# Optimization experiments

Measured on AMD Instinct MI355X. Metric: run time of the kernel, lower is better.

The kernel has to match this reference:

```python
import jax, jax.numpy as jnp
import numpy as np

NUM_HEADS = 16
HEAD_SIZE = 64
D_MODEL = NUM_HEADS * HEAD_SIZE  # 1024


def setup_inputs() -> dict:
    key = jax.random.key(0)
    ks = jax.random.split(key, 12)
    B, S = 4, 2048
    q = jax.random.normal(ks[0], (B, S, D_MODEL), dtype=jnp.float32)
    k = jax.random.normal(ks[1], (B, S, D_MODEL), dtype=jnp.float32)
    v = jax.random.normal(ks[2], (B, S, D_MODEL), dtype=jnp.float32)
    w = jax.random.uniform(ks[3], (B, S), dtype=jnp.float32)
    scale = 1.0 / np.sqrt(D_MODEL)
    Wq = jax.random.normal(ks[4], (D_MODEL, D_MODEL), dtype=jnp.float32) * scale
    Wk = jax.random.normal(ks[5], (D_MODEL, D_MODEL), dtype=jnp.float32) * scale
    Wv = jax.random.normal(ks[6], (D_MODEL, D_MODEL), dtype=jnp.float32) * scale
    Wo = jax.random.normal(ks[7], (D_MODEL, D_MODEL), dtype=jnp.float32) * scale
    bq = jnp.zeros((D_MODEL,), jnp.float32)
    bk = jnp.zeros((D_MODEL,), jnp.float32)
    bv = jnp.zeros((D_MODEL,), jnp.float32)
    bo = jnp.zeros((D_MODEL,), jnp.float32)
    return {"q": q, "k": k, "v": v, "w": w,
            "Wq": Wq, "bq": bq, "Wk": Wk, "bk": bk,
            "Wv": Wv, "bv": bv, "Wo": Wo, "bo": bo}


def reference(q, k, v, w, Wq, bq, Wk, bk, Wv, bv, Wo, bo):
    B, S, _ = q.shape
    H, Dh = NUM_HEADS, HEAD_SIZE

    def split_heads(x):  # [B,S,D] -> [B,H,S,Dh]
        return x.reshape(B, -1, H, Dh).transpose(0, 2, 1, 3)

    q_h = split_heads(q @ Wq + bq)
    k_h = split_heads(k @ Wk + bk)
    v_h = split_heads(v @ Wv + bv)

    # [B,H,Sq,Sk]
    score = jnp.einsum('bhqd,bhkd->bhqk', q_h, k_h) / jnp.sqrt(
        jnp.asarray(Dh, jnp.float32))
    # weighted unnormalized softmax: exp(score)*w / sum (no max subtraction,
    # faithful to original)
    exp_score = jnp.exp(score) * w[:, None, None, :]
    attn = exp_score / (jnp.sum(exp_score, axis=-1, keepdims=True) + 1e-12)

    context = jnp.einsum('bhqk,bhkd->bhqd', attn, v_h)  # [B,H,S,Dh]
    context = context.transpose(0, 2, 1, 3).reshape(B, -1, H * Dh)
    return context @ Wo + bo
```

## Files before the change

### kernel.cpp

```cpp
#include <hip/hip_runtime.h>
#include <hip/hip_bf16.h>

typedef __bf16 bf16x8 __attribute__((ext_vector_type(8)));
typedef float f32x4 __attribute__((ext_vector_type(4)));
typedef float f32x16 __attribute__((ext_vector_type(16)));
typedef unsigned short u16;
typedef unsigned int u32;

#define SB 4
#define SS 2048
#define SD 1024
#define SH 16
#define SDH 64

__device__ __forceinline__ u16 f2bf(float f) {
  union { float f; u32 u; } x; x.f = f;
  u32 r = (x.u + 0x7FFFu + ((x.u >> 16) & 1u)) >> 16;
  return (u16)r;
}

__device__ __forceinline__ void gl_lds16(const void* g, void* l) {
  __builtin_amdgcn_global_load_lds(
      (__attribute__((address_space(1))) void*)g,
      (__attribute__((address_space(3))) void*)l, 16, 0, 0);
}

__global__ void cast_bf16_kernel(const float* __restrict__ in,
                                 u32* __restrict__ out, int n8) {
  int i = blockIdx.x * blockDim.x + threadIdx.x;
  if (i >= n8) return;
  const float4* inp = (const float4*)in;
  float4 a = inp[2 * i], b = inp[2 * i + 1];
  uint4 o;
  o.x = (u32)f2bf(a.x) | ((u32)f2bf(a.y) << 16);
  o.y = (u32)f2bf(a.z) | ((u32)f2bf(a.w) << 16);
  o.z = (u32)f2bf(b.x) | ((u32)f2bf(b.y) << 16);
  o.w = (u32)f2bf(b.z) | ((u32)f2bf(b.w) << 16);
  ((uint4*)out)[i] = o;
}

__global__ void transpose_cast_kernel(const float* __restrict__ W,
                                      u16* __restrict__ Wt) {
  __shared__ float t[32][33];
  int bx = blockIdx.x, by = blockIdx.y;
  int tx = threadIdx.x, ty = threadIdx.y;
#pragma unroll
  for (int j = 0; j < 32; j += 8)
    t[ty + j][tx] = W[(size_t)(by * 32 + ty + j) * SD + bx * 32 + tx];
  __syncthreads();
#pragma unroll
  for (int j = 0; j < 32; j += 8)
    Wt[(size_t)(bx * 32 + ty + j) * SD + by * 32 + tx] = f2bf(t[tx][ty + j]);
}

template <int MODE>
__global__ __launch_bounds__(256, 2)
void gemm_bt(const u16* __restrict__ A, const u16* __restrict__ Bt,
             const float* __restrict__ bias, void* __restrict__ Out,
             int M, int N, int K) {
  __shared__ u16 Asl[2][128 * 64];
  __shared__ u16 Bsl[2][128 * 64];
  const int ntile = N >> 7;
  int bid = blockIdx.x;
  bid = (bid & 7) * ((int)gridDim.x >> 3) + (bid >> 3);
  int m0 = (bid / ntile) * 128, n0 = (bid % ntile) * 128;
  int tid = threadIdx.x;
  int lane = tid & 63, wv = tid >> 6;
  int wr = wv >> 1, wc = wv & 1;

  auto stage = [&](int buf, int k0) {
#pragma unroll
    for (int it = 0; it < 4; ++it) {
      int c = tid + it * 256;
      int row = c >> 3, sl = c & 7;
      int ssl = sl ^ (row & 7);
      gl_lds16(A + (size_t)(m0 + row) * K + k0 + ssl * 8,
               (char*)&Asl[buf][0] + c * 16);
      gl_lds16(Bt + (size_t)(n0 + row) * K + k0 + ssl * 8,
               (char*)&Bsl[buf][0] + c * 16);
    }
  };

  f32x4 acc[4][4] = {};
  stage(0, 0);
  asm volatile("s_waitcnt vmcnt(0)" ::: "memory");
  __syncthreads();

  int nk = K >> 6;
  for (int kt = 0; kt < nk; ++kt) {
    int buf = kt & 1;
    if (kt + 1 < nk) stage(buf ^ 1, (kt + 1) << 6);
#pragma unroll
    for (int kk = 0; kk < 2; ++kk) {
      bf16x8 af[4], bfr[4];
#pragma unroll
      for (int i = 0; i < 4; ++i) {
        int ar = wr * 64 + i * 16 + (lane & 15);
        int abyt = (ar * 128 + (kk * 32 + (lane >> 4) * 8) * 2) ^
                   ((ar & 7) << 4);
        af[i] = *(const bf16x8*)((const char*)&Asl[buf][0] + abyt);
        int br = wc * 64 + i * 16 + (lane & 15);
        int bbyt = (br * 128 + (kk * 32 + (lane >> 4) * 8) * 2) ^
                   ((br & 7) << 4);
        bfr[i] = *(const bf16x8*)((const char*)&Bsl[buf][0] + bbyt);
      }
#pragma unroll
      for (int i = 0; i < 4; ++i)
#pragma unroll
        for (int j = 0; j < 4; ++j)
          acc[i][j] = __builtin_amdgcn_mfma_f32_16x16x32_bf16(
              af[i], bfr[j], acc[i][j], 0, 0, 0);
    }
    asm volatile("s_waitcnt vmcnt(0)" ::: "memory");
    __syncthreads();
  }

  int cg = lane >> 4, cc = lane & 15;
#pragma unroll
  for (int i = 0; i < 4; ++i) {
#pragma unroll
    for (int j = 0; j < 4; ++j) {
#pragma unroll
      for (int r = 0; r < 4; ++r) {
        int m = m0 + wr * 64 + i * 16 + cg * 4 + r;
        int n = n0 + wc * 64 + j * 16 + cc;
        float val = acc[i][j][r];
        if (MODE == 0) {
          val = (val + bias[n]) * 0.18033688011112042f;
          int b = m >> 11, s = m & 2047, h = n >> 6, dh = n & 63;
          ((u16*)Out)[((size_t)((b * SH + h) * SS + s) << 6) + dh] = f2bf(val);
        } else if (MODE == 1) {
          val += bias[n];
          int b = m >> 11, s = m & 2047, h = n >> 6, dh = n & 63;
          ((u16*)Out)[((size_t)((b * SH + h) * SS + s) << 6) + dh] = f2bf(val);
        } else if (MODE == 2) {
          val += bias[m];
          int h = m >> 6, dh = m & 63, b = n >> 11, s = n & 2047;
          ((u16*)Out)[((size_t)((b * SH + h) * SDH + dh) << 11) + s] = f2bf(val);
        } else {
          val += bias[n];
          ((float*)Out)[(size_t)m * N + n] = val;
        }
      }
    }
  }
}

__global__ __launch_bounds__(256, 2)
void attn_kernel(const u16* __restrict__ Qh, const u16* __restrict__ Kh,
                 const u16* __restrict__ Vt, const float* __restrict__ w,
                 u16* __restrict__ Ctx) {
  __shared__ u16 Kl[2][8192];
  __shared__ u16 Vl[2][8192];
  __shared__ float wl[SS];

  int bid = blockIdx.x;
  int swz = (bid & 7) * 64 + (bid >> 3);
  int bh = swz >> 3;
  int qt = swz & 7;
  int b = bh >> 4, hh = bh & 15;
  int q0 = qt * 256;
  int tid = threadIdx.x, lane = tid & 63, wv = tid >> 6;
  int ql = lane & 31, h = lane >> 5;
  const size_t basebh = (size_t)bh * (SS * SDH);

  auto stage = [&](int buf, int t) {
    int kv0 = t * 128;
#pragma unroll
    for (int it = 0; it < 4; ++it) {
      int c = tid + it * 256;
      int kr = c >> 3, ks = c & 7;
      gl_lds16(Kh + basebh + (size_t)(kv0 + kr) * SDH + (ks ^ (kr & 7)) * 8,
               (char*)&Kl[buf][0] + c * 16);
      int vr = c >> 4, vs = c & 15;
      gl_lds16(Vt + basebh + (size_t)vr * SS + kv0 + (vs ^ (vr & 7)) * 8,
               (char*)&Vl[buf][0] + c * 16);
    }
  };

  stage(0, 0);

  const float* wb = w + b * SS;
  for (int i = tid; i < SS; i += 256)
    wl[i] = __builtin_amdgcn_logf(wb[i]);

  bf16x8 qf[2][4];
#pragma unroll
  for (int u = 0; u < 2; ++u) {
    const u16* qp =
        Qh + basebh + (size_t)(q0 + wv * 64 + u * 32 + ql) * SDH + h * 8;
#pragma unroll
    for (int st = 0; st < 4; ++st) qf[u][st] = *(const bf16x8*)(qp + st * 16);
  }

  f32x16 ctx[2][2] = {};
  float rs[2] = {0.f, 0.f};

  asm volatile("s_waitcnt vmcnt(0)" ::: "memory");
  __syncthreads();

  for (int t = 0; t < 16; ++t) {
    int buf = t & 1;
    if (t + 1 < 16) stage(buf ^ 1, t + 1);
#pragma unroll
    for (int half = 0; half < 2; ++half) {
      const char* Kb = (const char*)&Kl[buf][half * 4096];
      const char* Vb = (const char*)&Vl[buf][0];
      int vc0 = half * 64;
      int kvb = t * 128 + half * 64;
      u32 pk[2][8][2];
#pragma unroll
      for (int kt = 0; kt < 2; ++kt) {
        bf16x8 kf[4];
#pragma unroll
        for (int st = 0; st < 4; ++st) {
          int krow = kt * 32 + ql;
          int byt = (krow * 128 + (st * 16 + h * 8) * 2) ^ ((krow & 7) << 4);
          kf[st] = *(const bf16x8*)(Kb + byt);
        }
        float4 lw[4];
#pragma unroll
        for (int e2 = 0; e2 < 4; ++e2)
          lw[e2] = *(const float4*)&wl[kvb + kt * 32 + e2 * 8 + h * 4];
#pragma unroll
        for (int u = 0; u < 2; ++u) {
          f32x16 sc;
#pragma unroll
          for (int e2 = 0; e2 < 4; ++e2) {
            sc[e2 * 4 + 0] = lw[e2].x;
            sc[e2 * 4 + 1] = lw[e2].y;
            sc[e2 * 4 + 2] = lw[e2].z;
            sc[e2 * 4 + 3] = lw[e2].w;
          }
          __builtin_amdgcn_s_setprio(1);
#pragma unroll
          for (int st = 0; st < 4; ++st)
            sc = __builtin_amdgcn_mfma_f32_32x32x16_bf16(kf[st], qf[u][st],
                                                         sc, 0, 0, 0);
          __builtin_amdgcn_s_setprio(0);
#pragma unroll
          for (int e2 = 0; e2 < 4; ++e2) {
            float v0 = __builtin_amdgcn_exp2f(sc[e2 * 4 + 0]);
            float v1 = __builtin_amdgcn_exp2f(sc[e2 * 4 + 1]);
            float v2 = __builtin_amdgcn_exp2f(sc[e2 * 4 + 2]);
            float v3 = __builtin_amdgcn_exp2f(sc[e2 * 4 + 3]);
            rs[u] += (v0 + v1) + (v2 + v3);
            u32 p0, p1;
            asm("v_cvt_pk_bf16_f32 %0, %1, %2" : "=v"(p0) : "v"(v0), "v"(v1));
            asm("v_cvt_pk_bf16_f32 %0, %1, %2" : "=v"(p1) : "v"(v2), "v"(v3));
            pk[u][kt * 4 + e2][0] = p0;
            pk[u][kt * 4 + e2][1] = p1;
          }
        }
      }
#pragma unroll
      for (int ksl = 0; ksl < 4; ++ksl) {
        int cb = (vc0 + ksl * 16 + h * 8) * 2;
        int byt0 = (ql * 256 + cb) ^ ((ql & 7) << 4);
        bf16x8 vf0 = *(const bf16x8*)(Vb + byt0);
        int vr1 = 32 + ql;
        int byt1 = (vr1 * 256 + cb) ^ ((vr1 & 7) << 4);
        bf16x8 vf1 = *(const bf16x8*)(Vb + byt1);
#pragma unroll
        for (int u = 0; u < 2; ++u) {
          u32 d0 = pk[u][2 * ksl][0], d1 = pk[u][2 * ksl][1];
          u32 s0 = pk[u][2 * ksl + 1][0], s1 = pk[u][2 * ksl + 1][1];
          asm("v_permlane32_swap_b32 %0, %1" : "+v"(d0), "+v"(s0));
          asm("v_permlane32_swap_b32 %0, %1" : "+v"(d1), "+v"(s1));
          union { u32 uu[4]; bf16x8 v; } pa;
          pa.uu[0] = d0; pa.uu[1] = d1; pa.uu[2] = s0; pa.uu[3] = s1;
          __builtin_amdgcn_s_setprio(1);
          ctx[u][0] = __builtin_amdgcn_mfma_f32_32x32x16_bf16(
              pa.v, vf0, ctx[u][0], 0, 0, 0);
          ctx[u][1] = __builtin_amdgcn_mfma_f32_32x32x16_bf16(
              pa.v, vf1, ctx[u][1], 0, 0, 0);
          __builtin_amdgcn_s_setprio(0);
        }
      }
    }
    asm volatile("s_waitcnt vmcnt(0)" ::: "memory");
    __syncthreads();
  }

#pragma unroll
  for (int u = 0; u < 2; ++u) {
    float rsu = rs[u];
    rsu += __shfl_xor(rsu, 32, 64);
    float rinv = 1.0f / (rsu + 1e-12f);
#pragma unroll
    for (int reg = 0; reg < 16; ++reg) {
      int qrow = (reg & 3) + 8 * (reg >> 2) + 4 * h;
      float ri = __shfl(rinv, qrow, 64);
      int srow = q0 + wv * 64 + u * 32 + qrow;
      size_t base = ((size_t)(b * SS + srow) << 10) + hh * SDH;
      Ctx[base + ql] = f2bf(ctx[u][0][reg] * ri);
      Ctx[base + 32 + ql] = f2bf(ctx[u][1][reg] * ri);
    }
  }
}

extern "C" void kernel_launch(void* const* d_in, const int* in_sizes, int n_in,
                              void* d_out, int out_size, void* d_ws,
                              size_t ws_size, hipStream_t stream) {
  const float* q = (const float*)d_in[0];
  const float* k = (const float*)d_in[1];
  const float* v = (const float*)d_in[2];
  const float* w = (const float*)d_in[3];
  const float* Wq = (const float*)d_in[4];
  const float* bq = (const float*)d_in[5];
  const float* Wk = (const float*)d_in[6];
  const float* bk = (const float*)d_in[7];
  const float* Wv = (const float*)d_in[8];
  const float* bv = (const float*)d_in[9];
  const float* Wo = (const float*)d_in[10];
  const float* bo = (const float*)d_in[11];
  float* out = (float*)d_out;

  char* ws = (char*)d_ws;
  const size_t SZ = (size_t)8192 * 1024 * 2;
  u16* qb = (u16*)(ws);
  u16* kb = (u16*)(ws + SZ);
  u16* vb = (u16*)(ws + 2 * SZ);
  u16* WqT = (u16*)(ws + 3 * SZ);
  u16* WkT = WqT + 1024 * 1024;
  u16* WvT = WkT + 1024 * 1024;
  u16* WoT = WvT + 1024 * 1024;
  u16* Qh = (u16*)(ws + 3 * SZ + (size_t)4 * 1024 * 1024 * 2);
  u16* Kh = Qh + (size_t)8192 * 1024;
  u16* Vt = Kh + (size_t)8192 * 1024;
  u16* Ctx = qb;

  cast_bf16_kernel<<<4096, 256, 0, stream>>>(q, (u32*)qb, 1048576);
  cast_bf16_kernel<<<4096, 256, 0, stream>>>(k, (u32*)kb, 1048576);
  cast_bf16_kernel<<<4096, 256, 0, stream>>>(v, (u32*)vb, 1048576);

  dim3 tb(32, 8), tg(32, 32);
  transpose_cast_kernel<<<tg, tb, 0, stream>>>(Wq, WqT);
  transpose_cast_kernel<<<tg, tb, 0, stream>>>(Wk, WkT);
  transpose_cast_kernel<<<tg, tb, 0, stream>>>(Wv, WvT);
  transpose_cast_kernel<<<tg, tb, 0, stream>>>(Wo, WoT);

  gemm_bt<0><<<512, 256, 0, stream>>>(qb, WqT, bq, Qh, 8192, 1024, 1024);
  gemm_bt<1><<<512, 256, 0, stream>>>(kb, WkT, bk, Kh, 8192, 1024, 1024);
  gemm_bt<2><<<512, 256, 0, stream>>>(WvT, vb, bv, Vt, 1024, 8192, 1024);

  attn_kernel<<<512, 256, 0, stream>>>(Qh, Kh, Vt, w, Ctx);

  gemm_bt<3><<<512, 256, 0, stream>>>(Ctx, WoT, bo, out, 8192, 1024, 1024);
}
```

Measured before the change: 215.5 us.

## Load K/V fragments directly from global into registers, dropping LDS staging

Removes the LDS double-buffered K/V staging and its per-tile barriers. Each wave now loads its K and V MFMA fragments straight from global memory into registers, ping-ponging two register sets so the next tile's loads overlap the current tile's compute. This cuts LDS traffic and synchronisation, but each of the four waves now fetches the same K/V data separately, relying on L1/L2 to serve the duplicates. Register pressure also rises with two full fragment sets live at once.

```diff
diff --git a/kernel.cpp b/kernel.cpp
--- a/kernel.cpp
+++ b/kernel.cpp
@@ -150,8 +150,6 @@
 void attn_kernel(const u16* __restrict__ Qh, const u16* __restrict__ Kh,
                  const u16* __restrict__ Vt, const float* __restrict__ w,
                  u16* __restrict__ Ctx) {
-  __shared__ u16 Kl[2][8192];
-  __shared__ u16 Vl[2][8192];
   __shared__ float wl[SS];
 
   int bid = blockIdx.x;
@@ -163,26 +161,8 @@
   int tid = threadIdx.x, lane = tid & 63, wv = tid >> 6;
   int ql = lane & 31, h = lane >> 5;
   const size_t basebh = (size_t)bh * (SS * SDH);
-
-  auto stage = [&](int buf, int t) {
-    int kv0 = t * 128;
-#pragma unroll
-    for (int it = 0; it < 4; ++it) {
-      int c = tid + it * 256;
-      int kr = c >> 3, ks = c & 7;
-      gl_lds16(Kh + basebh + (size_t)(kv0 + kr) * SDH + (ks ^ (kr & 7)) * 8,
-               (char*)&Kl[buf][0] + c * 16);
-      int vr = c >> 4, vs = c & 15;
-      gl_lds16(Vt + basebh + (size_t)vr * SS + kv0 + (vs ^ (vr & 7)) * 8,
-               (char*)&Vl[buf][0] + c * 16);
-    }
-  };
-
-  stage(0, 0);
-
-  const float* wb = w + b * SS;
-  for (int i = tid; i < SS; i += 256)
-    wl[i] = __builtin_amdgcn_logf(wb[i]);
+  const u16* Kb = Kh + basebh + (size_t)ql * SDH + h * 8;
+  const u16* Vb = Vt + basebh + (size_t)ql * SS + h * 8;
 
   bf16x8 qf[2][4];
 #pragma unroll
@@ -193,93 +173,106 @@
     for (int st = 0; st < 4; ++st) qf[u][st] = *(const bf16x8*)(qp + st * 16);
   }
 
+  auto loadK = [&](bf16x8 (&kf)[2][4], int t) {
+    const u16* p = Kb + (size_t)t * 64 * SDH;
+#pragma unroll
+    for (int kt = 0; kt < 2; ++kt)
+#pragma unroll
+      for (int st = 0; st < 4; ++st)
+        kf[kt][st] = *(const bf16x8*)(p + kt * 32 * SDH + st * 16);
+  };
+  auto loadV = [&](bf16x8 (&vf)[4][2], int t) {
+    const u16* p = Vb + t * 64;
+#pragma unroll
+    for (int ksl = 0; ksl < 4; ++ksl)
+#pragma unroll
+      for (int vr = 0; vr < 2; ++vr)
+        vf[ksl][vr] = *(const bf16x8*)(p + (size_t)vr * 32 * SS + ksl * 16);
+  };
+
   f32x16 ctx[2][2] = {};
   float rs[2] = {0.f, 0.f};
 
-  asm volatile("s_waitcnt vmcnt(0)" ::: "memory");
-  __syncthreads();
-
-  for (int t = 0; t < 16; ++t) {
-    int buf = t & 1;
-    if (t + 1 < 16) stage(buf ^ 1, t + 1);
-#pragma unroll
-    for (int half = 0; half < 2; ++half) {
-      const char* Kb = (const char*)&Kl[buf][half * 4096];
-      const char* Vb = (const char*)&Vl[buf][0];
-      int vc0 = half * 64;
-      int kvb = t * 128 + half * 64;
-      u32 pk[2][8][2];
-#pragma unroll
-      for (int kt = 0; kt < 2; ++kt) {
-        bf16x8 kf[4];
-#pragma unroll
-        for (int st = 0; st < 4; ++st) {
-          int krow = kt * 32 + ql;
-          int byt = (krow * 128 + (st * 16 + h * 8) * 2) ^ ((krow & 7) << 4);
-          kf[st] = *(const bf16x8*)(Kb + byt);
+  auto compute = [&](const bf16x8 (&kf)[2][4], const bf16x8 (&vf)[4][2],
+                     int t) {
+    int kvb = t * 64;
+#pragma unroll
+    for (int kt = 0; kt < 2; ++kt) {
+      float4 lw[4];
+#pragma unroll
+      for (int e2 = 0; e2 < 4; ++e2)
+        lw[e2] = *(const float4*)&wl[kvb + kt * 32 + e2 * 8 + h * 4];
+      u32 pk[2][4][2];
+#pragma unroll
+      for (int u = 0; u < 2; ++u) {
+        f32x16 sc;
+#pragma unroll
+        for (int e2 = 0; e2 < 4; ++e2) {
+          sc[e2 * 4 + 0] = lw[e2].x;
+          sc[e2 * 4 + 1] = lw[e2].y;
+          sc[e2 * 4 + 2] = lw[e2].z;
+          sc[e2 * 4 + 3] = lw[e2].w;
         }
-        float4 lw[4];
-#pragma unroll
-        for (int e2 = 0; e2 < 4; ++e2)
-          lw[e2] = *(const float4*)&wl[kvb + kt * 32 + e2 * 8 + h * 4];
-#pragma unroll
-        for (int u = 0; u < 2; ++u) {
-          f32x16 sc;
-#pragma unroll
-          for (int e2 = 0; e2 < 4; ++e2) {
-            sc[e2 * 4 + 0] = lw[e2].x;
-            sc[e2 * 4 + 1] = lw[e2].y;
-            sc[e2 * 4 + 2] = lw[e2].z;
-            sc[e2 * 4 + 3] = lw[e2].w;
-          }
-          __builtin_amdgcn_s_setprio(1);
-#pragma unroll
-          for (int st = 0; st < 4; ++st)
-            sc = __builtin_amdgcn_mfma_f32_32x32x16_bf16(kf[st], qf[u][st],
-                                                         sc, 0, 0, 0);
-          __builtin_amdgcn_s_setprio(0);
-#pragma unroll
-          for (int e2 = 0; e2 < 4; ++e2) {
-            float v0 = __builtin_amdgcn_exp2f(sc[e2 * 4 + 0]);
-            float v1 = __builtin_amdgcn_exp2f(sc[e2 * 4 + 1]);
-            float v2 = __builtin_amdgcn_exp2f(sc[e2 * 4 + 2]);
-            float v3 = __builtin_amdgcn_exp2f(sc[e2 * 4 + 3]);
-            rs[u] += (v0 + v1) + (v2 + v3);
-            u32 p0, p1;
-            asm("v_cvt_pk_bf16_f32 %0, %1, %2" : "=v"(p0) : "v"(v0), "v"(v1));
-            asm("v_cvt_pk_bf16_f32 %0, %1, %2" : "=v"(p1) : "v"(v2), "v"(v3));
-            pk[u][kt * 4 + e2][0] = p0;
-            pk[u][kt * 4 + e2][1] = p1;
-          }
+        __builtin_amdgcn_s_setprio(1);
+#pragma unroll
+        for (int st = 0; st < 4; ++st)
+          sc = __builtin_amdgcn_mfma_f32_32x32x16_bf16(kf[kt][st], qf[u][st],
+                                                       sc, 0, 0, 0);
+        __builtin_amdgcn_s_setprio(0);
+#pragma unroll
+        for (int e2 = 0; e2 < 4; ++e2) {
+          float v0 = __builtin_amdgcn_exp2f(sc[e2 * 4 + 0]);
+          float v1 = __builtin_amdgcn_exp2f(sc[e2 * 4 + 1]);
+          float v2 = __builtin_amdgcn_exp2f(sc[e2 * 4 + 2]);
+          float v3 = __builtin_amdgcn_exp2f(sc[e2 * 4 + 3]);
+          rs[u] += (v0 + v1) + (v2 + v3);
+          u32 p0, p1;
+          asm("v_cvt_pk_bf16_f32 %0, %1, %2" : "=v"(p0) : "v"(v0), "v"(v1));
+          asm("v_cvt_pk_bf16_f32 %0, %1, %2" : "=v"(p1) : "v"(v2), "v"(v3));
+          pk[u][e2][0] = p0;
+          pk[u][e2][1] = p1;
         }
       }
 #pragma unroll
-      for (int ksl = 0; ksl < 4; ++ksl) {
-        int cb = (vc0 + ksl * 16 + h * 8) * 2;
-        int byt0 = (ql * 256 + cb) ^ ((ql & 7) << 4);
-        bf16x8 vf0 = *(const bf16x8*)(Vb + byt0);
-        int vr1 = 32 + ql;
-        int byt1 = (vr1 * 256 + cb) ^ ((vr1 & 7) << 4);
-        bf16x8 vf1 = *(const bf16x8*)(Vb + byt1);
+      for (int ksl2 = 0; ksl2 < 2; ++ksl2) {
+        int ksl = kt * 2 + ksl2;
 #pragma unroll
         for (int u = 0; u < 2; ++u) {
-          u32 d0 = pk[u][2 * ksl][0], d1 = pk[u][2 * ksl][1];
-          u32 s0 = pk[u][2 * ksl + 1][0], s1 = pk[u][2 * ksl + 1][1];
+          u32 d0 = pk[u][2 * ksl2][0], d1 = pk[u][2 * ksl2][1];
+          u32 s0 = pk[u][2 * ksl2 + 1][0], s1 = pk[u][2 * ksl2 + 1][1];
           asm("v_permlane32_swap_b32 %0, %1" : "+v"(d0), "+v"(s0));
           asm("v_permlane32_swap_b32 %0, %1" : "+v"(d1), "+v"(s1));
           union { u32 uu[4]; bf16x8 v; } pa;
           pa.uu[0] = d0; pa.uu[1] = d1; pa.uu[2] = s0; pa.uu[3] = s1;
           __builtin_amdgcn_s_setprio(1);
           ctx[u][0] = __builtin_amdgcn_mfma_f32_32x32x16_bf16(
-              pa.v, vf0, ctx[u][0], 0, 0, 0);
+              pa.v, vf[ksl][0], ctx[u][0], 0, 0, 0);
           ctx[u][1] = __builtin_amdgcn_mfma_f32_32x32x16_bf16(
-              pa.v, vf1, ctx[u][1], 0, 0, 0);
+              pa.v, vf[ksl][1], ctx[u][1], 0, 0, 0);
           __builtin_amdgcn_s_setprio(0);
         }
       }
     }
-    asm volatile("s_waitcnt vmcnt(0)" ::: "memory");
-    __syncthreads();
+  };
+
+  bf16x8 kA[2][4], vA[4][2], kB[2][4], vB[4][2];
+  loadK(kA, 0);
+  loadV(vA, 0);
+
+  const float* wb = w + b * SS;
+  for (int i = tid; i < SS; i += 256)
+    wl[i] = __builtin_amdgcn_logf(wb[i]);
+  __syncthreads();
+
+  for (int t = 0; t < 32; t += 2) {
+    loadK(kB, t + 1);
+    loadV(vB, t + 1);
+    compute(kA, vA, t);
+    if (t + 2 < 32) {
+      loadK(kA, t + 2);
+      loadV(vA, t + 2);
+    }
+    compute(kB, vB, t + 1);
   }
 
 #pragma unroll
```

Measured after the change: 434.4 us. 2.02x slower.
